# Performance work log

Hardware: AMD Instinct MI355X
Metric: run time of the kernel (lower is better)

The kernel has to match this reference:

```python
import jax, jax.numpy as jnp
import numpy as np

B, S, H = 2, 2048, 2048
NH, HD = 32, 64            # num heads, head dim (H = NH*HD)
FFN = 8192
EPS = 1e-5


def _layernorm(x, g, b):
    mu = jnp.mean(x, axis=-1, keepdims=True)
    var = jnp.mean(jnp.square(x - mu), axis=-1, keepdims=True)
    return (x - mu) * jax.lax.rsqrt(var + EPS) * g + b


def setup_inputs() -> dict:
    key = jax.random.key(0)
    ks = jax.random.split(key, 8)
    s = lambda fan_in: 1.0 / np.sqrt(fan_in)
    return {
        "x": jax.random.normal(ks[0], (B, S, H), dtype=jnp.float32),
        "ln1_g": jnp.ones((H,), jnp.float32),
        "ln1_b": jnp.zeros((H,), jnp.float32),
        "w_qkv": jax.random.normal(ks[1], (H, 3 * H), jnp.float32) * s(H),
        "b_qkv": jnp.zeros((3 * H,), jnp.float32),
        "w_proj": jax.random.normal(ks[2], (H, H), jnp.float32) * s(H),
        "b_proj": jnp.zeros((H,), jnp.float32),
        "ln2_g": jnp.ones((H,), jnp.float32),
        "ln2_b": jnp.zeros((H,), jnp.float32),
        "w1": jax.random.normal(ks[3], (H, FFN), jnp.float32) * s(H),
        "b1": jnp.zeros((FFN,), jnp.float32),
        "w2": jax.random.normal(ks[4], (FFN, H), jnp.float32) * s(FFN),
        "b2": jnp.zeros((H,), jnp.float32),
    }


def reference(x, ln1_g, ln1_b, w_qkv, b_qkv, w_proj, b_proj,
              ln2_g, ln2_b, w1, b1, w2, b2):
    # Pre-LN attention block (dropout in eval mode -> identity)
    res = x
    h = _layernorm(x, ln1_g, ln1_b)
    qkv = h @ w_qkv + b_qkv                       # [B,S,3H]
    qkv = qkv.reshape(B, S, NH, 3 * HD)           # matches tf reshape+split on axis 3
    q, k, v = jnp.split(qkv, 3, axis=3)           # each [B,S,NH,HD]
    scores = jnp.einsum('bqhd,bkhd->bhqk', q, k) / jnp.sqrt(jnp.float32(HD))
    probs = jax.nn.softmax(scores, axis=-1)       # [B,NH,S,S]
    ctx = jnp.einsum('bhqk,bkhd->bqhd', probs, v).reshape(B, S, H)
    x = ctx @ w_proj + b_proj
    x = res + x
    # Pre-LN MLP block
    res = x
    h = _layernorm(x, ln2_g, ln2_b)
    h = jax.nn.gelu(h @ w1 + b1, approximate=True)
    h = h @ w2 + b2
    return h + res
```

## Files before the change

kernel.cpp:

```cpp
#include <hip/hip_runtime.h>
#include <hip/hip_bf16.h>
#include <math.h>


typedef __attribute__((ext_vector_type(8))) short bf16x8;
typedef __attribute__((ext_vector_type(4))) float f32x4;
typedef __attribute__((ext_vector_type(16))) float f32x16;

#define DEV __device__ __forceinline__

static constexpr int SEQ  = 2048;
static constexpr int HID  = 2048;
static constexpr int NHEAD = 32;
static constexpr int HDIM = 64;
static constexpr int NFFN = 8192;
static constexpr int NTOK = 2 * SEQ;
static constexpr int QKVW = 3 * HID;

#define QSCALE 0.1803368801111204f

#if defined(__has_builtin)
#if __has_builtin(__builtin_amdgcn_exp2f)
#define EXP2(x) __builtin_amdgcn_exp2f(x)
#endif
#endif
#ifndef EXP2
#define EXP2(x) exp2f(x)
#endif

#define VMCNT(n) asm volatile("s_waitcnt vmcnt(" #n ")" ::: "memory")

DEV ushort f2bf(float f) {
  unsigned u = __float_as_uint(f);
  return (ushort)((u + 0x7fffu + ((u >> 16) & 1u)) >> 16);
}

DEV void gload16(const void* g, void* l) {
  __builtin_amdgcn_global_load_lds(
      (const __attribute__((address_space(1))) unsigned int*)g,
      (__attribute__((address_space(3))) unsigned int*)l, 16, 0, 0);
}

__global__ __launch_bounds__(256) void tcvt_kernel(const float* __restrict__ in,
                                                   ushort* __restrict__ out,
                                                   int R, int C) {
  __shared__ ushort tile[64][72];
  const int tr = blockIdx.y * 64, tc = blockIdx.x * 64;
  const int t = threadIdx.x;
  const int rr = t >> 2, c4 = (t & 3) * 16;
  const float4* ip = (const float4*)(in + (size_t)(tr + rr) * C + tc + c4);
  float4 a0 = ip[0], a1 = ip[1], a2 = ip[2], a3 = ip[3];
  ushort* tp = &tile[rr][c4];
  tp[0]=f2bf(a0.x); tp[1]=f2bf(a0.y); tp[2]=f2bf(a0.z); tp[3]=f2bf(a0.w);
  tp[4]=f2bf(a1.x); tp[5]=f2bf(a1.y); tp[6]=f2bf(a1.z); tp[7]=f2bf(a1.w);
  tp[8]=f2bf(a2.x); tp[9]=f2bf(a2.y); tp[10]=f2bf(a2.z); tp[11]=f2bf(a2.w);
  tp[12]=f2bf(a3.x); tp[13]=f2bf(a3.y); tp[14]=f2bf(a3.z); tp[15]=f2bf(a3.w);
  __syncthreads();
  union { ushort u[8]; bf16x8 v; } p0, p1;
#pragma unroll
  for (int j = 0; j < 8; ++j) { p0.u[j] = tile[c4 + j][rr]; p1.u[j] = tile[c4 + 8 + j][rr]; }
  ushort* op = out + (size_t)(tc + rr) * R + tr + c4;
  *(bf16x8*)op = p0.v;
  *(bf16x8*)(op + 8) = p1.v;
}

__global__ __launch_bounds__(256) void ln_kernel(const float* __restrict__ x,
                                                 const float* __restrict__ g,
                                                 const float* __restrict__ bb,
                                                 ushort* __restrict__ out) {
  const int row = blockIdx.x, t = threadIdx.x;
  const float4* xv = (const float4*)(x + (size_t)row * HID);
  float4 a0 = xv[t * 2], a1 = xv[t * 2 + 1];
  float s  = a0.x + a0.y + a0.z + a0.w + a1.x + a1.y + a1.z + a1.w;
  float ss = a0.x*a0.x + a0.y*a0.y + a0.z*a0.z + a0.w*a0.w
           + a1.x*a1.x + a1.y*a1.y + a1.z*a1.z + a1.w*a1.w;
#pragma unroll
  for (int o = 32; o > 0; o >>= 1) { s += __shfl_down(s, o); ss += __shfl_down(ss, o); }
  __shared__ float red[8];
  const int w = t >> 6, l = t & 63;
  if (l == 0) { red[w] = s; red[4 + w] = ss; }
  __syncthreads();
  s  = red[0] + red[1] + red[2] + red[3];
  ss = red[4] + red[5] + red[6] + red[7];
  const float mu = s * (1.f / HID);
  const float rs = rsqrtf(ss * (1.f / HID) - mu * mu + 1e-5f);
  const float4* gv = (const float4*)g;
  const float4* bv = (const float4*)bb;
  float4 g0 = gv[t * 2], g1 = gv[t * 2 + 1], b0 = bv[t * 2], b1 = bv[t * 2 + 1];
  union { ushort u[8]; bf16x8 v; } p;
  p.u[0] = f2bf((a0.x - mu) * rs * g0.x + b0.x);
  p.u[1] = f2bf((a0.y - mu) * rs * g0.y + b0.y);
  p.u[2] = f2bf((a0.z - mu) * rs * g0.z + b0.z);
  p.u[3] = f2bf((a0.w - mu) * rs * g0.w + b0.w);
  p.u[4] = f2bf((a1.x - mu) * rs * g1.x + b1.x);
  p.u[5] = f2bf((a1.y - mu) * rs * g1.y + b1.y);
  p.u[6] = f2bf((a1.z - mu) * rs * g1.z + b1.z);
  p.u[7] = f2bf((a1.w - mu) * rs * g1.w + b1.w);
  *(bf16x8*)(out + (size_t)row * HID + t * 8) = p.v;
}

DEV void qkv_store(int row, int col, float v,
                   ushort* __restrict__ qpk, ushort* __restrict__ kpk,
                   ushort* __restrict__ vpk) {
  const int h = col / 192;
  const int c = col - h * 192;
  const int bh2 = (row >> 11) * 32 + h;
  const int t32 = (row >> 5) & 63;
  const int r5 = row & 31;
  if (c < 64) {
    const int s = c >> 4, hi2 = (c >> 3) & 1, j = c & 7;
    qpk[(((size_t)bh2 * 64 + t32) * 4 + s) * 512 + (hi2 * 32 + r5) * 8 + j] = f2bf(v * QSCALE);
  } else if (c < 128) {
    const int d = c - 64;
    const int s = d >> 4, hi2 = (d >> 3) & 1, j = d & 7;
    kpk[(((size_t)bh2 * 64 + t32) * 4 + s) * 512 + (hi2 * 32 + r5) * 8 + j] = f2bf(v);
  } else {
    const int d = c - 128;
    const int ks = r5 >> 4, hi2 = (r5 >> 3) & 1, j = r5 & 7;
    const int half = d >> 5, dl = d & 31;
    vpk[((((size_t)bh2 * 64 + t32) * 2 + ks) * 2 + half) * 512 + (hi2 * 32 + dl) * 8 + j] = f2bf(v);
  }
}

DEV bf16x8 ldsfrag(const char* base, int row, int slot) {
  return *(const bf16x8*)(base + row * 128 + (((slot ^ (row & 7)) << 4)));
}

template <int BM>
DEV void stageA(const ushort* __restrict__ A, int Kd, int tm, int kt,
                char* abuf, int w, int lr, int lsl, int mh, int s) {
  int row;
  if (BM == 256) {
    row = s * 128 + mh * 64 + w * 8 + lr;
  } else {
    const int ri = w * 8 + lr;
    row = (ri >> 5) * 64 + mh * 32 + (ri & 31);
  }
  gload16(A + (size_t)(tm + row) * Kd + kt + ((lsl ^ lr) << 3),
          abuf + row * 128 + lsl * 16);
}

DEV void stageB(const ushort* __restrict__ BT, int Kd, int tn, int kt,
                char* bbuf, int w, int lr, int lsl, int nh, int s) {
  const int ri = s * 64 + w * 8 + lr;
  const int row = (ri >> 5) * 64 + nh * 32 + (ri & 31);
  gload16(BT + (size_t)(tn + row) * Kd + kt + ((lsl ^ lr) << 3),
          bbuf + row * 128 + lsl * 16);
}

template <int BM>
DEV void ktile(const ushort* __restrict__ A, const ushort* __restrict__ BT,
               int K, int tm, int tn,
               const char* CA, const char* CB, char* NA, char* NB,
               int ktn, bool dost, int w, int l, f32x4 (&acc)[BM / 32][4]) {
  constexpr int MH = BM / 64;
  const int l16 = l & 15, lg = l >> 4, lr = l >> 3, lsl = l & 7;
  const int wm = w >> 2, wn = w & 3;
  bf16x8 af[MH][2];
#pragma unroll
  for (int q = 0; q < 4; ++q) {
    const int mh = q >> 1, nh = q & 1;
    if ((q & 1) == 0) {
#pragma unroll
      for (int mi = 0; mi < MH; ++mi)
#pragma unroll
        for (int ks = 0; ks < 2; ++ks)
          af[mi][ks] = ldsfrag(CA, wm * (BM / 2) + mh * (BM / 4) + mi * 16 + l16, ks * 4 + lg);
    }
    bf16x8 bfr[2][2];
#pragma unroll
    for (int ni = 0; ni < 2; ++ni)
#pragma unroll
      for (int ks = 0; ks < 2; ++ks)
        bfr[ni][ks] = ldsfrag(CB, wn * 64 + nh * 32 + ni * 16 + l16, ks * 4 + lg);
    if (dost && q < 2) {
      stageA<BM>(A, K, tm, ktn, NA, w, lr, lsl, q, 0);
      if (BM == 256) stageA<BM>(A, K, tm, ktn, NA, w, lr, lsl, q, 1);
      stageB(BT, K, tn, ktn, NB, w, lr, lsl, q, 0);
      stageB(BT, K, tn, ktn, NB, w, lr, lsl, q, 1);
    }
    if (q == 0) {
      if (dost) { if (BM == 256) VMCNT(4); else VMCNT(3); }
      else VMCNT(0);
    }
    if (q == 3 && dost) { if (BM == 256) VMCNT(4); else VMCNT(3); }
    __builtin_amdgcn_s_barrier();
    asm volatile("s_waitcnt lgkmcnt(0)" ::: "memory");
    __builtin_amdgcn_sched_barrier(0);
    __builtin_amdgcn_s_setprio(1);
#pragma unroll
    for (int mi = 0; mi < MH; ++mi)
#pragma unroll
      for (int ni = 0; ni < 2; ++ni)
#pragma unroll
        for (int ks = 0; ks < 2; ++ks)
          acc[mh * MH + mi][nh * 2 + ni] = __builtin_amdgcn_mfma_f32_16x16x32_bf16(
              af[mi][ks], bfr[ni][ks], acc[mh * MH + mi][nh * 2 + ni], 0, 0, 0);
    __builtin_amdgcn_s_setprio(0);
  }
}

template <int BM, int EPI>
__global__ __launch_bounds__(512, 2) void gemm8p_kernel(
    const ushort* __restrict__ A, const ushort* __restrict__ BT,
    const float* __restrict__ bias, const float* __restrict__ res,
    void* __restrict__ outv,
    ushort* __restrict__ qpk, ushort* __restrict__ kpk, ushort* __restrict__ vpk,
    int M, int N, int K, int RH, int RW) {
  constexpr int MR = BM / 32;

  __shared__ ushort lds[2 * (BM * 64 + 256 * 64)];
  char* const a0p = (char*)lds;
  char* const b0p = a0p + BM * 128;
  char* const a1p = b0p + 32768;
  char* const b1p = a1p + BM * 128;

  const int t = threadIdx.x;
  const int w = t >> 6, l = t & 63;
  const int l16 = l & 15, lg = l >> 4;
  const int lr = l >> 3, lsl = l & 7;
  const int wm = w >> 2, wn = w & 3;

  const int lin = blockIdx.y * gridDim.x + blockIdx.x;
  const int xcd = lin & 7, loc = lin >> 3;
  const int nrw = gridDim.x / RW;
  const int bm = (xcd / nrw) * RH + (loc % RH);
  const int bn = (xcd % nrw) * RW + (loc / RH);
  const int tm = bm * BM, tn = bn * 256;

  const f32x4 z4 = {0.f, 0.f, 0.f, 0.f};
  f32x4 acc[MR][4];
#pragma unroll
  for (int i = 0; i < MR; ++i)
#pragma unroll
    for (int j = 0; j < 4; ++j) acc[i][j] = z4;

#pragma unroll
  for (int mh = 0; mh < 2; ++mh) {
    stageA<BM>(A, K, tm, 0, a0p, w, lr, lsl, mh, 0);
    if (BM == 256) stageA<BM>(A, K, tm, 0, a0p, w, lr, lsl, mh, 1);
    stageB(BT, K, tn, 0, b0p, w, lr, lsl, mh, 0);
    stageB(BT, K, tn, 0, b0p, w, lr, lsl, mh, 1);
  }
  VMCNT(0);
  __builtin_amdgcn_s_barrier();

  const int nt = K >> 6;
  for (int it = 0; it < nt; it += 2) {
    ktile<BM>(A, BT, K, tm, tn, a0p, b0p, a1p, b1p, (it + 1) << 6, true, w, l, acc);
    ktile<BM>(A, BT, K, tm, tn, a1p, b1p, a0p, b0p, (it + 2) << 6, (it + 2) < nt, w, l, acc);
  }

  const int row0 = tm + wm * (BM / 2) + lg * 4;
  const int col0 = tn + wn * 64 + l16;
#pragma unroll
  for (int ni = 0; ni < 4; ++ni) {
    const int col = col0 + ni * 16;
    const float bvl = bias[col];
#pragma unroll
    for (int mi = 0; mi < MR; ++mi) {
#pragma unroll
      for (int r = 0; r < 4; ++r) {
        const int row = row0 + mi * 16 + r;
        float v = acc[mi][ni][r] + bvl;
        if (EPI == 1) {
          const size_t off = (size_t)row * N + col;
          ((float*)outv)[off] = v + res[off];
        } else if (EPI == 2) {
          const float u = 0.7978845608f * (v + 0.044715f * v * v * v);
          ((ushort*)outv)[(size_t)row * N + col] = f2bf(v / (1.f + __expf(-2.f * u)));
        } else if (EPI == 3) {
          qkv_store(row, col, v, qpk, kpk, vpk);
        } else {
          ((ushort*)outv)[(size_t)row * N + col] = f2bf(v);
        }
      }
    }
  }
}

__global__ __launch_bounds__(256) void attn_kernel(const ushort* __restrict__ qpk,
                                                   const ushort* __restrict__ kpk,
                                                   const ushort* __restrict__ vpk,
                                                   ushort* __restrict__ ctx) {
  const int lin = blockIdx.x + blockIdx.y * gridDim.x;
  const int work = (lin & 7) * 128 + (lin >> 3);
  const int qt = work & 15, bh = work >> 4;
  const int b = bh >> 5, h = bh & 31;
  const int t = threadIdx.x, w = t >> 6, l = t & 63;
  const int l32 = l & 31, hi = l >> 5;

  const ushort* qb = qpk + ((((size_t)bh * 64 + qt * 4 + w) * 4) * 64 + l) * 8;
  bf16x8 qf0 = *(const bf16x8*)(qb);
  bf16x8 qf1 = *(const bf16x8*)(qb + 512);
  bf16x8 qf2 = *(const bf16x8*)(qb + 1024);
  bf16x8 qf3 = *(const bf16x8*)(qb + 1536);

  const ushort* kbase = kpk + (size_t)bh * 131072 + l * 8;
  const ushort* vbase = vpk + (size_t)bh * 131072 + l * 8;

  f32x16 oacc0, oacc1;
#pragma unroll
  for (int r = 0; r < 16; ++r) { oacc0[r] = 0.f; oacc1[r] = 0.f; }
  float m = -1e30f, lsum = 0.f;
  const f32x16 z16 = {};

#define LOADK(k0, k1, k2, k3, kt) {                                           \
    const ushort* p_ = kbase + (size_t)(kt) * 2048;                           \
    k0 = *(const bf16x8*)(p_);        k1 = *(const bf16x8*)(p_ + 512);        \
    k2 = *(const bf16x8*)(p_ + 1024); k3 = *(const bf16x8*)(p_ + 1536); }
#define LOADV(v0, v1, v2, v3, kt) {                                           \
    const ushort* p_ = vbase + (size_t)(kt) * 2048;                           \
    v0 = *(const bf16x8*)(p_);        v1 = *(const bf16x8*)(p_ + 512);        \
    v2 = *(const bf16x8*)(p_ + 1024); v3 = *(const bf16x8*)(p_ + 1536); }

#define STEP(k0, k1, k2, k3, v0, v1, v2, v3) {                                \
    f32x16 s = __builtin_amdgcn_mfma_f32_32x32x16_bf16(k0, qf0, z16, 0, 0, 0);\
    s = __builtin_amdgcn_mfma_f32_32x32x16_bf16(k1, qf1, s, 0, 0, 0);         \
    s = __builtin_amdgcn_mfma_f32_32x32x16_bf16(k2, qf2, s, 0, 0, 0);         \
    s = __builtin_amdgcn_mfma_f32_32x32x16_bf16(k3, qf3, s, 0, 0, 0);         \
    float tm_ = s[0];                                                         \
    _Pragma("unroll") for (int r = 1; r < 16; ++r) tm_ = fmaxf(tm_, s[r]);    \
    tm_ = fmaxf(tm_, __shfl_xor(tm_, 32));                                    \
    if (!__all(tm_ - m <= 8.f)) {                                             \
      const float mn = fmaxf(m, tm_);                                         \
      const float sf = EXP2(m - mn);                                          \
      m = mn;                                                                 \
      lsum *= sf;                                                             \
      _Pragma("unroll") for (int r = 0; r < 16; ++r) {                        \
        const float f = __shfl(sf, (r & 3) + 8 * (r >> 2) + 4 * hi);          \
        oacc0[r] *= f; oacc1[r] *= f;                                         \
      }                                                                       \
    }                                                                         \
    float p[16];                                                              \
    _Pragma("unroll") for (int r = 0; r < 16; ++r) p[r] = EXP2(s[r] - m);     \
    float ls = 0.f;                                                           \
    _Pragma("unroll") for (int r = 0; r < 16; ++r) ls += p[r];                \
    lsum += ls;                                                               \
    unsigned pw[8];                                                           \
    _Pragma("unroll") for (int i = 0; i < 8; ++i)                             \
      asm("v_cvt_pk_bf16_f32 %0, %1, %2" : "=v"(pw[i]) : "v"(p[2*i]), "v"(p[2*i+1])); \
    unsigned a0 = pw[0], b0 = pw[2];                                          \
    asm("v_permlane32_swap_b32 %0, %1" : "+v"(a0), "+v"(b0));                 \
    unsigned a1 = pw[1], b1 = pw[3];                                          \
    asm("v_permlane32_swap_b32 %0, %1" : "+v"(a1), "+v"(b1));                 \
    unsigned a2 = pw[4], b2 = pw[6];                                          \
    asm("v_permlane32_swap_b32 %0, %1" : "+v"(a2), "+v"(b2));                 \
    unsigned a3 = pw[5], b3 = pw[7];                                          \
    asm("v_permlane32_swap_b32 %0, %1" : "+v"(a3), "+v"(b3));                 \
    union { unsigned uw[4]; bf16x8 v; } pa0, pa1;                             \
    pa0.uw[0] = a0; pa0.uw[1] = a1; pa0.uw[2] = b0; pa0.uw[3] = b1;           \
    pa1.uw[0] = a2; pa1.uw[1] = a3; pa1.uw[2] = b2; pa1.uw[3] = b3;           \
    oacc0 = __builtin_amdgcn_mfma_f32_32x32x16_bf16(pa0.v, v0, oacc0, 0, 0, 0);\
    oacc1 = __builtin_amdgcn_mfma_f32_32x32x16_bf16(pa0.v, v1, oacc1, 0, 0, 0);\
    oacc0 = __builtin_amdgcn_mfma_f32_32x32x16_bf16(pa1.v, v2, oacc0, 0, 0, 0);\
    oacc1 = __builtin_amdgcn_mfma_f32_32x32x16_bf16(pa1.v, v3, oacc1, 0, 0, 0);}

  bf16x8 ka0, ka1, ka2, ka3, kc0, kc1, kc2, kc3;
  LOADK(ka0, ka1, ka2, ka3, 0);
  for (int kt = 0; kt < 64; kt += 2) {
    bf16x8 va0, va1, va2, va3;
    LOADV(va0, va1, va2, va3, kt);
    LOADK(kc0, kc1, kc2, kc3, kt + 1);
    STEP(ka0, ka1, ka2, ka3, va0, va1, va2, va3);
    LOADV(va0, va1, va2, va3, kt + 1);
    if (kt + 2 < 64) LOADK(ka0, ka1, ka2, ka3, kt + 2);
    STEP(kc0, kc1, kc2, kc3, va0, va1, va2, va3);
  }
#undef LOADK
#undef LOADV
#undef STEP

  const float lf = lsum + __shfl_xor(lsum, 32);
  const float linv = 1.f / lf;
#pragma unroll
  for (int r = 0; r < 16; ++r) {
    const int qr = (r & 3) + 8 * (r >> 2);
    const float fac = __shfl(linv, qr + 4 * hi);
    const int row = qt * 128 + w * 32 + qr + 4 * hi;
    const size_t base = ((size_t)(b * SEQ + row)) * HID + h * 64 + l32;
    ctx[base]      = f2bf(oacc0[r] * fac);
    ctx[base + 32] = f2bf(oacc1[r] * fac);
  }
}

extern "C" void kernel_launch(void* const* d_in, const int* in_sizes, int n_in,
                              void* d_out, int out_size, void* d_ws, size_t ws_size,
                              hipStream_t stream) {
  const float* x      = (const float*)d_in[0];
  const float* ln1g   = (const float*)d_in[1];
  const float* ln1b   = (const float*)d_in[2];
  const float* w_qkv  = (const float*)d_in[3];
  const float* b_qkv  = (const float*)d_in[4];
  const float* w_proj = (const float*)d_in[5];
  const float* b_proj = (const float*)d_in[6];
  const float* ln2g   = (const float*)d_in[7];
  const float* ln2b   = (const float*)d_in[8];
  const float* w1     = (const float*)d_in[9];
  const float* b1     = (const float*)d_in[10];
  const float* w2     = (const float*)d_in[11];
  const float* b2     = (const float*)d_in[12];

  char* ws = (char*)d_ws;
  ushort* wqkvT  = (ushort*)(ws + 0);
  ushort* wprojT = (ushort*)(ws + 25165824);
  ushort* w1T    = (ushort*)(ws + 33554432);
  ushort* w2T    = (ushort*)(ws + 67108864);
  ushort* hbuf   = (ushort*)(ws + 100663296);
  ushort* qpk    = (ushort*)(ws + 117440512);
  ushort* kpk    = (ushort*)(ws + 134217728);
  ushort* vpk    = (ushort*)(ws + 150994944);
  ushort* ctxb   = (ushort*)(ws + 167772160);
  ushort* gelu   = (ushort*)(ws + 117440512);
  float*  x2     = (float*)(ws + 184549376);

  tcvt_kernel<<<dim3(96, 32),  256, 0, stream>>>(w_qkv,  wqkvT, 2048, 6144);
  tcvt_kernel<<<dim3(32, 32),  256, 0, stream>>>(w_proj, wprojT, 2048, 2048);
  tcvt_kernel<<<dim3(128, 32), 256, 0, stream>>>(w1,     w1T,   2048, 8192);
  tcvt_kernel<<<dim3(32, 128), 256, 0, stream>>>(w2,     w2T,   8192, 2048);

  ln_kernel<<<NTOK, 256, 0, stream>>>(x, ln1g, ln1b, hbuf);
  gemm8p_kernel<128, 3><<<dim3(24, 32), 512, 0, stream>>>(
      hbuf, wqkvT, b_qkv, nullptr, nullptr, qpk, kpk, vpk, NTOK, QKVW, HID, 16, 6);
  attn_kernel<<<dim3(16, 2 * NHEAD), 256, 0, stream>>>(qpk, kpk, vpk, ctxb);
  gemm8p_kernel<128, 1><<<dim3(8, 32), 512, 0, stream>>>(
      ctxb, wprojT, b_proj, x, x2, nullptr, nullptr, nullptr, NTOK, HID, HID, 8, 4);
  ln_kernel<<<NTOK, 256, 0, stream>>>(x2, ln2g, ln2b, hbuf);
  gemm8p_kernel<256, 2><<<dim3(32, 16), 512, 0, stream>>>(
      hbuf, w1T, b1, nullptr, gelu, nullptr, nullptr, nullptr, NTOK, NFFN, HID, 8, 8);
  gemm8p_kernel<128, 1><<<dim3(8, 32), 512, 0, stream>>>(
      gelu, w2T, b2, x2, (float*)d_out, nullptr, nullptr, nullptr, NTOK, HID, NFFN, 8, 4);
}
```

Before: 640.4 us.

## Switch GEMM mainloop to 32x32x16 MFMA with software-pipelined LDS fragment reads

Replaces the 16x16x32 MFMA tiles in the shared GEMM kernel with 32x32x16 MFMA, which reads fewer LDS fragments per FLOP and changes the accumulator layout. The k-tile loop is restructured so the four k-slices use ping-pong register fragments: the next slice's LDS reads are issued while the current slice's MFMAs run, gated by partial lgkmcnt waits. Global prefetch is now issued all at once per tile, with a single vmcnt(0) and one barrier at the end instead of per-quarter barriers. The epilogue row mapping is rewritten for the 32x32 output layout. Waiting for all global loads at the end of every tile may expose more load latency.

```diff
diff --git a/kernel.cpp b/kernel.cpp
--- a/kernel.cpp
+++ b/kernel.cpp
@@ -29,6 +29,8 @@
 #endif
 
 #define VMCNT(n) asm volatile("s_waitcnt vmcnt(" #n ")" ::: "memory")
+#define LGKM(n)  asm volatile("s_waitcnt lgkmcnt(" #n ")" ::: "memory")
+#define SB0()    __builtin_amdgcn_sched_barrier(0)
 
 DEV ushort f2bf(float f) {
   unsigned u = __float_as_uint(f);
@@ -122,9 +124,6 @@
   }
 }
 
-DEV bf16x8 ldsfrag(const char* base, int row, int slot) {
-  return *(const bf16x8*)(base + row * 128 + (((slot ^ (row & 7)) << 4)));
-}
 
 template <int BM>
 DEV void stageA(const ushort* __restrict__ A, int Kd, int tm, int kt,
@@ -149,55 +148,73 @@
 }
 
 template <int BM>
-DEV void ktile(const ushort* __restrict__ A, const ushort* __restrict__ BT,
-               int K, int tm, int tn,
-               const char* CA, const char* CB, char* NA, char* NB,
-               int ktn, bool dost, int w, int l, f32x4 (&acc)[BM / 32][4]) {
-  constexpr int MH = BM / 64;
-  const int l16 = l & 15, lg = l >> 4, lr = l >> 3, lsl = l & 7;
+DEV void rdfrags(const char* CA, const char* CB, int ks, int wm, int wn,
+                 int l32, int hi, bf16x8 (&af)[BM / 64], bf16x8 (&bf)[2]) {
+  const int slot = ks * 2 + hi;
+#pragma unroll
+  for (int mi = 0; mi < BM / 64; ++mi) {
+    const int row = wm * (BM / 2) + mi * 32 + l32;
+    af[mi] = *(const bf16x8*)(CA + row * 128 + ((slot ^ (row & 7)) << 4));
+  }
+#pragma unroll
+  for (int ni = 0; ni < 2; ++ni) {
+    const int row = wn * 64 + ni * 32 + l32;
+    bf[ni] = *(const bf16x8*)(CB + row * 128 + ((slot ^ (row & 7)) << 4));
+  }
+}
+
+template <int BM>
+DEV void domfma(bf16x8 (&af)[BM / 64], bf16x8 (&bf)[2], f32x16 (&acc)[BM / 64][2]) {
+  __builtin_amdgcn_s_setprio(1);
+#pragma unroll
+  for (int mi = 0; mi < BM / 64; ++mi)
+#pragma unroll
+    for (int ni = 0; ni < 2; ++ni)
+      acc[mi][ni] = __builtin_amdgcn_mfma_f32_32x32x16_bf16(af[mi], bf[ni], acc[mi][ni], 0, 0, 0);
+  __builtin_amdgcn_s_setprio(0);
+}
+
+template <int BM>
+DEV void tile32(const ushort* __restrict__ A, const ushort* __restrict__ BT,
+                int K, int tm, int tn,
+                const char* CA, const char* CB, char* NA, char* NB,
+                int ktn, bool dost, int w, int l, f32x16 (&acc)[BM / 64][2]) {
+  constexpr int MT = BM / 64;
+  const int l32 = l & 31, hi = l >> 5, lr = l >> 3, lsl = l & 7;
   const int wm = w >> 2, wn = w & 3;
-  bf16x8 af[MH][2];
-#pragma unroll
-  for (int q = 0; q < 4; ++q) {
-    const int mh = q >> 1, nh = q & 1;
-    if ((q & 1) == 0) {
-#pragma unroll
-      for (int mi = 0; mi < MH; ++mi)
-#pragma unroll
-        for (int ks = 0; ks < 2; ++ks)
-          af[mi][ks] = ldsfrag(CA, wm * (BM / 2) + mh * (BM / 4) + mi * 16 + l16, ks * 4 + lg);
+  bf16x8 aE[MT], bE[2], aO[MT], bO[2];
+  rdfrags<BM>(CA, CB, 0, wm, wn, l32, hi, aE, bE);
+  SB0();
+  rdfrags<BM>(CA, CB, 1, wm, wn, l32, hi, aO, bO);
+  SB0();
+  if (dost) {
+#pragma unroll
+    for (int mh = 0; mh < 2; ++mh) {
+      stageA<BM>(A, K, tm, ktn, NA, w, lr, lsl, mh, 0);
+      if (BM == 256) stageA<BM>(A, K, tm, ktn, NA, w, lr, lsl, mh, 1);
+      stageB(BT, K, tn, ktn, NB, w, lr, lsl, mh, 0);
+      stageB(BT, K, tn, ktn, NB, w, lr, lsl, mh, 1);
     }
-    bf16x8 bfr[2][2];
-#pragma unroll
-    for (int ni = 0; ni < 2; ++ni)
-#pragma unroll
-      for (int ks = 0; ks < 2; ++ks)
-        bfr[ni][ks] = ldsfrag(CB, wn * 64 + nh * 32 + ni * 16 + l16, ks * 4 + lg);
-    if (dost && q < 2) {
-      stageA<BM>(A, K, tm, ktn, NA, w, lr, lsl, q, 0);
-      if (BM == 256) stageA<BM>(A, K, tm, ktn, NA, w, lr, lsl, q, 1);
-      stageB(BT, K, tn, ktn, NB, w, lr, lsl, q, 0);
-      stageB(BT, K, tn, ktn, NB, w, lr, lsl, q, 1);
-    }
-    if (q == 0) {
-      if (dost) { if (BM == 256) VMCNT(4); else VMCNT(3); }
-      else VMCNT(0);
-    }
-    if (q == 3 && dost) { if (BM == 256) VMCNT(4); else VMCNT(3); }
-    __builtin_amdgcn_s_barrier();
-    asm volatile("s_waitcnt lgkmcnt(0)" ::: "memory");
-    __builtin_amdgcn_sched_barrier(0);
-    __builtin_amdgcn_s_setprio(1);
-#pragma unroll
-    for (int mi = 0; mi < MH; ++mi)
-#pragma unroll
-      for (int ni = 0; ni < 2; ++ni)
-#pragma unroll
-        for (int ks = 0; ks < 2; ++ks)
-          acc[mh * MH + mi][nh * 2 + ni] = __builtin_amdgcn_mfma_f32_16x16x32_bf16(
-              af[mi][ks], bfr[ni][ks], acc[mh * MH + mi][nh * 2 + ni], 0, 0, 0);
-    __builtin_amdgcn_s_setprio(0);
-  }
+  }
+  if (BM == 256) { LGKM(6); } else { LGKM(4); }
+  SB0();
+  domfma<BM>(aE, bE, acc);
+  rdfrags<BM>(CA, CB, 2, wm, wn, l32, hi, aE, bE);
+  SB0();
+  if (BM == 256) { LGKM(6); } else { LGKM(4); }
+  SB0();
+  domfma<BM>(aO, bO, acc);
+  rdfrags<BM>(CA, CB, 3, wm, wn, l32, hi, aO, bO);
+  SB0();
+  if (BM == 256) { LGKM(6); } else { LGKM(4); }
+  SB0();
+  domfma<BM>(aE, bE, acc);
+  LGKM(0);
+  SB0();
+  domfma<BM>(aO, bO, acc);
+  if (dost) VMCNT(0);
+  __builtin_amdgcn_s_barrier();
+  asm volatile("" ::: "memory");
 }
 
 template <int BM, int EPI>
@@ -207,7 +224,7 @@
     void* __restrict__ outv,
     ushort* __restrict__ qpk, ushort* __restrict__ kpk, ushort* __restrict__ vpk,
     int M, int N, int K, int RH, int RW) {
-  constexpr int MR = BM / 32;
+  constexpr int MT = BM / 64;
 
   __shared__ ushort lds[2 * (BM * 64 + 256 * 64)];
   char* const a0p = (char*)lds;
@@ -217,7 +234,7 @@
 
   const int t = threadIdx.x;
   const int w = t >> 6, l = t & 63;
-  const int l16 = l & 15, lg = l >> 4;
+  const int l32 = l & 31, hi = l >> 5;
   const int lr = l >> 3, lsl = l & 7;
   const int wm = w >> 2, wn = w & 3;
 
@@ -228,12 +245,13 @@
   const int bn = (xcd % nrw) * RW + (loc / RH);
   const int tm = bm * BM, tn = bn * 256;
 
-  const f32x4 z4 = {0.f, 0.f, 0.f, 0.f};
-  f32x4 acc[MR][4];
-#pragma unroll
-  for (int i = 0; i < MR; ++i)
-#pragma unroll
-    for (int j = 0; j < 4; ++j) acc[i][j] = z4;
+  f32x16 acc[MT][2];
+#pragma unroll
+  for (int i = 0; i < MT; ++i)
+#pragma unroll
+    for (int j = 0; j < 2; ++j)
+#pragma unroll
+      for (int r = 0; r < 16; ++r) acc[i][j][r] = 0.f;
 
 #pragma unroll
   for (int mh = 0; mh < 2; ++mh) {
@@ -244,24 +262,23 @@
   }
   VMCNT(0);
   __builtin_amdgcn_s_barrier();
+  asm volatile("" ::: "memory");
 
   const int nt = K >> 6;
   for (int it = 0; it < nt; it += 2) {
-    ktile<BM>(A, BT, K, tm, tn, a0p, b0p, a1p, b1p, (it + 1) << 6, true, w, l, acc);
-    ktile<BM>(A, BT, K, tm, tn, a1p, b1p, a0p, b0p, (it + 2) << 6, (it + 2) < nt, w, l, acc);
-  }
-
-  const int row0 = tm + wm * (BM / 2) + lg * 4;
-  const int col0 = tn + wn * 64 + l16;
-#pragma unroll
-  for (int ni = 0; ni < 4; ++ni) {
-    const int col = col0 + ni * 16;
+    tile32<BM>(A, BT, K, tm, tn, a0p, b0p, a1p, b1p, (it + 1) << 6, true, w, l, acc);
+    tile32<BM>(A, BT, K, tm, tn, a1p, b1p, a0p, b0p, (it + 2) << 6, (it + 2) < nt, w, l, acc);
+  }
+
+#pragma unroll
+  for (int ni = 0; ni < 2; ++ni) {
+    const int col = tn + wn * 64 + ni * 32 + l32;
     const float bvl = bias[col];
 #pragma unroll
-    for (int mi = 0; mi < MR; ++mi) {
-#pragma unroll
-      for (int r = 0; r < 4; ++r) {
-        const int row = row0 + mi * 16 + r;
+    for (int mi = 0; mi < MT; ++mi) {
+#pragma unroll
+      for (int r = 0; r < 16; ++r) {
+        const int row = tm + wm * (BM / 2) + mi * 32 + (r & 3) + 8 * (r >> 2) + 4 * hi;
         float v = acc[mi][ni][r] + bvl;
         if (EPI == 1) {
           const size_t off = (size_t)row * N + col;
```

New measurement: 676.6 us. 1.06x slower.
